# Optimization experiments

Measured on AMD Instinct MI355X. Metric: run time of the kernel, lower is better.

Reference implementation:

```python
import jax, jax.numpy as jnp
import numpy as np

B, C, H, W = 4, 64, 160, 160
OUT = 64
KS = (5, 7)


def conv2d(x, w, b=None, pad=0, groups=1):
    y = jax.lax.conv_general_dilated(
        x, w, (1, 1), [(pad, pad), (pad, pad)],
        feature_group_count=groups,
        dimension_numbers=('NCHW', 'OIHW', 'NCHW'))
    return y if b is None else y + b[None, :, None, None]


def bn_eval(x, g, b, m, v, eps=1e-5):
    s = g / jnp.sqrt(v + eps)
    return x * s[None, :, None, None] + (b - m * s)[None, :, None, None]


def boundary_attn(x, w1, b1, w2, b2):
    Cc = x.shape[1]
    kx = jnp.array([[-1., 0., 1.], [-2., 0., 2.], [-1., 0., 1.]], jnp.float32)
    ky = jnp.array([[-1., -2., -1.], [0., 0., 0.], [1., 2., 1.]], jnp.float32)
    sobel = jnp.concatenate([jnp.tile(kx[None, None], (Cc, 1, 1, 1)),
                             jnp.tile(ky[None, None], (Cc, 1, 1, 1))], axis=0)  # [2C,1,3,3]
    # grouped conv (groups=C): same output-channel grouping semantics as torch
    edge = jnp.abs(conv2d(x, sobel, pad=1, groups=Cc))
    edge = (edge[:, :Cc] + edge[:, Cc:]).mean(axis=1, keepdims=True)
    a = jax.nn.relu(conv2d(x, w1, b1, pad=1))
    a = conv2d(a, w2, b2, pad=0)
    a = jax.nn.sigmoid(a + edge)
    return x * a + x


def icc(off, half_k):
    # iterative cumulative constraint over the (small, static) K channel axis
    K = off.shape[1]
    cs = [None] * K
    cs[half_k] = off[:, half_k]
    for i in range(1, half_k + 1):
        cs[half_k - i] = 0.5 * cs[half_k - i + 1] + 0.5 * off[:, half_k - i]
        cs[half_k + i] = 0.5 * cs[half_k + i - 1] + 0.5 * off[:, half_k + i]
    c = jnp.stack(cs, axis=1)
    w = jnp.ones((K, 1, 3, 3), jnp.float32) / 9.0
    return conv2d(c, w, pad=1, groups=K)


def tumor_center(x):
    _, _, Hx, Wx = x.shape
    fs = x.mean(axis=1)  # [B,H,W]
    hg = jnp.arange(Hx, dtype=x.dtype)[None, :, None]
    wg = jnp.arange(Wx, dtype=x.dtype)[None, None, :]
    tot = fs.sum(axis=(1, 2)) + 1e-6
    return (fs * hg).sum(axis=(1, 2)) / tot, (fs * wg).sum(axis=(1, 2)) / tot


def dyn1d(x, kw, kb, K, O):
    # Original Dynamic1DConv reshapes x to [B*H*W, C, 1, 1] and grid_samples a
    # [1,K] grid per pixel. With align_corners=True a 1x1 input maps every grid
    # coordinate to ix=iy=0, so sampled[n,c,k] == x[b,c,h,w] for all k; the
    # bmm with per-pixel kernels followed by sum over C therefore collapses to
    # (sum_c x) * (sum_k kernels) -- same math, no giant gather materialized.
    Bx, _, Hx, Wx = x.shape
    ker = conv2d(x, kw, kb, pad=0).reshape(Bx, O, K, Hx, Wx)
    return x.sum(axis=1, keepdims=True) * ker.sum(axis=2)


def reference(x, ba_w1, ba_b1, ba_w2, ba_b2,
              off_w1, off_b1, off_bn_g, off_bn_b, off_bn_m, off_bn_v,
              off_w2, off_b2,
              rk5_w, rk5_b, rk7_w, rk7_b,
              lk5_w, lk5_b, lk7_w, lk7_b,
              sf_w, sf_b, sf_bn_g, sf_bn_b, sf_bn_m, sf_bn_v,
              fc_w, fc_b):
    residual = x  # in_channels == out_channels -> nn.Identity
    xa = boundary_attn(x, ba_w1, ba_b1, ba_w2, ba_b2)
    # offset branch (faithful to original; mathematically dead because the
    # per-pixel grid_sample ignores its grid -- see dyn1d). BN in eval mode.
    raw = conv2d(xa, off_w1, off_b1, pad=1)
    raw = jax.nn.relu(bn_eval(raw, off_bn_g, off_bn_b, off_bn_m, off_bn_v))
    raw = conv2d(raw, off_w2, off_b2, pad=1)
    sumk, idx = sum(KS), 0
    _offs = []
    for k in KS:
        _offs.append(icc(jnp.tanh(raw[:, idx:idx + k]), k // 2))
        _offs.append(icc(jnp.tanh(raw[:, sumk + idx:sumk + idx + k]), k // 2))
        idx += k
    _hc, _wc = tumor_center(xa)  # also dead w.r.t. output
    O = OUT // 2 // len(KS)  # 16 channels per scale per flow type
    feats = [dyn1d(xa, rk5_w, rk5_b, 5, O), dyn1d(xa, rk7_w, rk7_b, 7, O),
             dyn1d(xa, lk5_w, lk5_b, 5, O), dyn1d(xa, lk7_w, lk7_b, 7, O)]
    fusion = jnp.concatenate(feats, axis=1)  # [B, OUT, H, W]
    y = jax.nn.relu(bn_eval(conv2d(fusion, sf_w, sf_b, pad=1),
                            sf_bn_g, sf_bn_b, sf_bn_m, sf_bn_v))
    y = conv2d(y, fc_w, fc_b, pad=0)
    return y + residual


def setup_inputs() -> dict:
    key = jax.random.key(0)
    keys = iter(jax.random.split(key, 40))
    def nrm(shape, s=0.05):
        return jax.random.normal(next(keys), shape, jnp.float32) * s
    d = {}
    d['x'] = nrm((B, C, H, W), 1.0)
    d['ba_w1'] = nrm((C // 2, C, 3, 3)); d['ba_b1'] = nrm((C // 2,))
    d['ba_w2'] = nrm((1, C // 2, 1, 1)); d['ba_b2'] = nrm((1,))
    d['off_w1'] = nrm((C // 2, C, 3, 3)); d['off_b1'] = nrm((C // 2,))
    d['off_bn_g'] = 1.0 + nrm((C // 2,)); d['off_bn_b'] = nrm((C // 2,))
    d['off_bn_m'] = nrm((C // 2,))
    d['off_bn_v'] = jax.random.uniform(next(keys), (C // 2,), jnp.float32, 0.5, 1.5)
    d['off_w2'] = nrm((2 * sum(KS), C // 2, 3, 3)); d['off_b2'] = nrm((2 * sum(KS),))
    O = OUT // 2 // len(KS)
    for name, k in (('rk5', 5), ('rk7', 7), ('lk5', 5), ('lk7', 7)):
        d[name + '_w'] = nrm((O * k, C, 1, 1)); d[name + '_b'] = nrm((O * k,))
    d['sf_w'] = nrm((OUT, OUT, 3, 3)); d['sf_b'] = nrm((OUT,))
    d['sf_bn_g'] = 1.0 + nrm((OUT,)); d['sf_bn_b'] = nrm((OUT,))
    d['sf_bn_m'] = nrm((OUT,))
    d['sf_bn_v'] = jax.random.uniform(next(keys), (OUT,), jnp.float32, 0.5, 1.5)
    d['fc_w'] = nrm((OUT, OUT, 1, 1)); d['fc_b'] = nrm((OUT,))
    return d
```

## Files before the change

kernel.cpp:

```cpp
#include <hip/hip_runtime.h>
#include <hip/hip_bf16.h>
#include <math.h>

#define BB 4
#define CC 64
#define HH 160
#define WW 160
#define HWs (HH*WW)
#define NPIX (BB*HWs)

using bf16 = __hip_bfloat16;
typedef __attribute__((ext_vector_type(8)))  short short8v;
typedef __attribute__((ext_vector_type(16))) float float16v;

__device__ __forceinline__ unsigned short f2bfu(float f){
    union { bf16 h; unsigned short u; } cv; cv.h = __float2bfloat16(f); return cv.u;
}
__device__ __forceinline__ float bfu2f(unsigned short u){
    union { float f; unsigned int i; } cv; cv.i = ((unsigned int)u)<<16; return cv.f;
}
__device__ __forceinline__ float16v fzero16(){
    float16v z;
    #pragma unroll
    for(int i=0;i<16;i++) z[i]=0.f;
    return z;
}

constexpr int B1X1 = 0;
constexpr int SFBo = 64;
constexpr int SFWf = 128;
constexpr int BAWf = 18560;
constexpr int FUWf = 27776;
constexpr int FCWf = 29824;
constexpr int WS_FLOATS = 31872;

__global__ void k_prep(const float* __restrict__ rk5w, const float* __restrict__ rk5b,
                       const float* __restrict__ rk7w, const float* __restrict__ rk7b,
                       const float* __restrict__ lk5w, const float* __restrict__ lk5b,
                       const float* __restrict__ lk7w, const float* __restrict__ lk7b,
                       const float* __restrict__ sfw,  const float* __restrict__ sfb,
                       const float* __restrict__ bng,  const float* __restrict__ bnb,
                       const float* __restrict__ bnm,  const float* __restrict__ bnv,
                       const float* __restrict__ baw1, const float* __restrict__ fcw,
                       float* __restrict__ ws)
{
    int tid = blockIdx.x*blockDim.x + threadIdx.x;
    int nt  = gridDim.x*blockDim.x;
    for(int o=tid;o<64;o+=nt){
        int grp=o>>4, oo=o&15; int K=(grp&1)?7:5;
        const float* bp = (grp==0)?rk5b:(grp==1)?rk7b:(grp==2)?lk5b:lk7b;
        float s=0.f; for(int k=0;k<K;k++) s += bp[oo*K+k];
        ws[B1X1+o]=s;
    }
    for(int oc=tid;oc<64;oc+=nt){
        float sc = bng[oc]*rsqrtf(bnv[oc]+1e-5f);
        ws[SFBo+oc] = sfb[oc]*sc + bnb[oc] - bnm[oc]*sc;
    }
    unsigned short* sfwf = (unsigned short*)(ws + SFWf);
    for(int idx=tid; idx<36864; idx+=nt){
        int og = idx/18432;  int rem = idx - og*18432;
        int f  = rem>>9;     int r2 = rem & 511;
        int lane = r2>>3;    int j = r2&7;
        int tap = f>>2, kc = f&3;
        int oc = og*32 + (lane&31);
        int ic = kc*16 + (lane>>5)*8 + j;
        float sc = bng[oc]*rsqrtf(bnv[oc]+1e-5f);
        sfwf[idx] = f2bfu(sfw[(oc*64+ic)*9 + tap] * sc);
    }
    unsigned short* bawf = (unsigned short*)(ws + BAWf);
    for(int idx=tid; idx<18432; idx+=nt){
        int f  = idx>>9;     int r2 = idx & 511;
        int lane = r2>>3;    int j = r2&7;
        int tap = f>>2, kc = f&3;
        int oc = lane&31;
        int ic = kc*16 + (lane>>5)*8 + j;
        bawf[idx] = f2bfu(baw1[(oc*64+ic)*9 + tap]);
    }
    unsigned short* fuwf = (unsigned short*)(ws + FUWf);
    for(int idx=tid; idx<4096; idx+=nt){
        int og   = idx>>11;
        int kc   = (idx>>9)&3;
        int lane = (idx>>3)&63;
        int j    = idx&7;
        int oc = og*32 + (lane&31);
        int c  = kc*16 + (lane>>5)*8 + j;
        int grp = oc>>4, oo = oc&15; int K = (grp&1)?7:5;
        const float* w = (grp==0)?rk5w:(grp==1)?rk7w:(grp==2)?lk5w:lk7w;
        float s = 0.f;
        for(int k=0;k<K;k++) s += w[(oo*K+k)*64 + c];
        fuwf[idx] = f2bfu(s);
    }
    unsigned short* fcwf = (unsigned short*)(ws + FCWf);
    for(int idx=tid; idx<4096; idx+=nt){
        int og   = idx>>11;
        int kc   = (idx>>9)&3;
        int lane = (idx>>3)&63;
        int j    = idx&7;
        int oc = og*32 + (lane&31);
        int c  = kc*16 + (lane>>5)*8 + j;
        fcwf[idx] = f2bfu(fcw[oc*64 + c]);
    }
}

__global__ __launch_bounds__(256)
void k_x2nhwc(const float* __restrict__ x, unsigned short* __restrict__ xb)
{
    __shared__ unsigned short ls[128*72];
    const int t = threadIdx.x;
    const int p0 = blockIdx.x*128;
    const int b = p0 / HWs, pp0 = p0 % HWs;
    const float4* xb4 = (const float4*)(x + (size_t)b*CC*HWs + pp0);
    #pragma unroll
    for(int iter=0; iter<8; iter++){
        int idx = iter*256 + t;
        int c = idx>>5, g = idx&31;
        float4 v = xb4[(size_t)c*(HWs/4) + g];
        int px = g*4;
        int bs = (c>>3) ^ ((g>>1)&7);
        unsigned short* base = ls + bs*8 + (c&7);
        base[(px+0)*72] = f2bfu(v.x);
        base[(px+1)*72] = f2bfu(v.y);
        base[(px+2)*72] = f2bfu(v.z);
        base[(px+3)*72] = f2bfu(v.w);
    }
    __syncthreads();
    #pragma unroll
    for(int iter=0; iter<4; iter++){
        int idx = iter*256 + t;
        int sub = idx&7, px = idx>>3;
        int bs = sub ^ ((px>>3)&7);
        short8v v = *(short8v*)(ls + px*72 + bs*8);
        *(short8v*)(xb + ((size_t)(p0+px))*64 + sub*8) = v;
    }
}

__global__ __launch_bounds__(512, 4)
void k_fuse(const unsigned short* __restrict__ xb, const float* __restrict__ bab1,
            const float* __restrict__ baw2, const float* __restrict__ bab2,
            const float* __restrict__ ws, const float* __restrict__ fcb,
            const float* __restrict__ x, float* __restrict__ out)
{
    __shared__ unsigned short xt[240*72];
    __shared__ unsigned short ftile[180*72];
    __shared__ float ebuf[2][180];
    const int bw = blockIdx.x, bh = blockIdx.y, b = blockIdx.z;
    const int t = threadIdx.x;
    const int wave = t>>6, lane = t&63;
    const int half = lane>>5, n = lane&31;
    const int w0 = bw*16, h0 = bh*8;

    const unsigned short* fb = xb + (size_t)b*HWs*64;
    for(int idx=t; idx<1920; idx+=512){
        int sub = idx&7; int pix = idx>>3;
        int r = pix/20, c = pix - r*20;
        int gh = h0-2+r, gw = w0-2+c;
        short8v v = {0,0,0,0,0,0,0,0};
        if(gh>=0&&gh<HH&&gw>=0&&gw<WW)
            v = *(const short8v*)(fb + ((size_t)(gh*WW+gw))*64 + sub*8);
        *(short8v*)(xt + pix*72 + sub*8) = v;
    }
    __syncthreads();

    float cz = 0.f, sx = 0.f;
    if(wave < 6){
        int p = wave*32 + n; if(p > 179) p = 179;
        int pr = p/18, pc = p - pr*18;
        const unsigned short* bawf = (const unsigned short*)(ws + BAWf);
        float16v acc = fzero16();
        #pragma unroll
        for(int kc=0; kc<4; kc++){
            short8v af[9];
            #pragma unroll
            for(int tap=0; tap<9; tap++)
                af[tap] = *(const short8v*)(bawf + (((size_t)(tap*4+kc))*64 + lane)*8);
            #pragma unroll
            for(int tap=0; tap<9; tap++){
                const int dh = tap/3, dw = tap%3;
                short8v bf = *(const short8v*)(xt + ((pr+dh)*20 + pc+dw)*72
                                               + kc*16 + half*8);
                acc = __builtin_amdgcn_mfma_f32_32x32x16_bf16(af[tap], bf, acc, 0,0,0);
            }
        }
        #pragma unroll
        for(int r=0;r<16;r++){
            int oc = (r&3) + 8*(r>>2) + 4*half;
            cz += fmaxf(acc[r]+bab1[oc],0.f)*baw2[oc];
        }
        cz += __shfl_xor(cz, 32);
        short8v ones;
        #pragma unroll
        for(int j=0;j<8;j++) ones[j] = (short)0x3F80;
        float16v s = fzero16();
        #pragma unroll
        for(int kc=0; kc<4; kc++){
            short8v bf = *(const short8v*)(xt + ((pr+1)*20 + pc+1)*72 + kc*16 + half*8);
            s = __builtin_amdgcn_mfma_f32_32x32x16_bf16(ones, bf, s, 0,0,0);
        }
        sx = s[0];
    }
    {
        const int i2 = 511 - t;
        if(i2 < 360){
            const int hf = (i2>=180) ? 1 : 0;
            const int px2 = i2 - hf*180;
            const int r = px2/18, c = px2 - (px2/18)*18;
            float e = 0.f;
            #pragma unroll
            for(int s=0; s<4; s++){
                const int sub = hf*4 + s;
                if(hf==0){
                    short8v a0 = *(const short8v*)(xt + ((r  )*20 + c  )*72 + sub*8);
                    short8v a2 = *(const short8v*)(xt + ((r  )*20 + c+2)*72 + sub*8);
                    short8v a3 = *(const short8v*)(xt + ((r+1)*20 + c  )*72 + sub*8);
                    short8v a5 = *(const short8v*)(xt + ((r+1)*20 + c+2)*72 + sub*8);
                    short8v a6 = *(const short8v*)(xt + ((r+2)*20 + c  )*72 + sub*8);
                    short8v a8 = *(const short8v*)(xt + ((r+2)*20 + c+2)*72 + sub*8);
                    #pragma unroll
                    for(int j=0;j<8;j++){
                        float gx = (bfu2f((unsigned short)a2[j]) - bfu2f((unsigned short)a0[j]))
                           + 2.f*(bfu2f((unsigned short)a5[j]) - bfu2f((unsigned short)a3[j]))
                           +      (bfu2f((unsigned short)a8[j]) - bfu2f((unsigned short)a6[j]));
                        e += fabsf(gx);
                    }
                } else {
                    short8v b0 = *(const short8v*)(xt + ((r  )*20 + c  )*72 + sub*8);
                    short8v b1 = *(const short8v*)(xt + ((r  )*20 + c+1)*72 + sub*8);
                    short8v b2 = *(const short8v*)(xt + ((r  )*20 + c+2)*72 + sub*8);
                    short8v b6 = *(const short8v*)(xt + ((r+2)*20 + c  )*72 + sub*8);
                    short8v b7 = *(const short8v*)(xt + ((r+2)*20 + c+1)*72 + sub*8);
                    short8v b8 = *(const short8v*)(xt + ((r+2)*20 + c+2)*72 + sub*8);
                    #pragma unroll
                    for(int j=0;j<8;j++){
                        float gy = (bfu2f((unsigned short)b6[j]) - bfu2f((unsigned short)b0[j]))
                           + 2.f*(bfu2f((unsigned short)b7[j]) - bfu2f((unsigned short)b1[j]))
                           +      (bfu2f((unsigned short)b2[j]) - bfu2f((unsigned short)b2[j]))*0.f
                           +      (bfu2f((unsigned short)b8[j]) - bfu2f((unsigned short)b2[j]));
                        e += fabsf(gy);
                    }
                }
            }
            ebuf[hf][px2] = e;
        }
    }
    __syncthreads();

    if(wave < 6){
        const unsigned short* fuwf = (const unsigned short*)(ws + FUWf);
        int p0g = wave*32 + n;
        bool wr = (p0g < 180);
        int p = wr ? p0g : 179;
        int pr = p/18, pc = p - pr*18;
        float z = cz + bab2[0] + (ebuf[0][p] + ebuf[1][p]) * (1.f/32.f);
        float A = 1.f + 1.f/(1.f+__expf(-z));
        float Q = A * sx;
        float P = A * Q;
        #pragma unroll
        for(int og=0; og<2; og++){
            float16v a = fzero16();
            #pragma unroll
            for(int kc=0; kc<4; kc++){
                short8v wf = *(const short8v*)(fuwf + (((size_t)og*4 + kc)*64 + lane)*8);
                short8v bf = *(const short8v*)(xt + ((pr+1)*20 + pc+1)*72 + kc*16 + half*8);
                a = __builtin_amdgcn_mfma_f32_32x32x16_bf16(wf, bf, a, 0,0,0);
            }
            float bq[16];
            #pragma unroll
            for(int r=0;r<16;r++) bq[r] = ws[B1X1 + og*32 + (r&3)+8*(r>>2)+4*half];
            unsigned short* base = ftile + p*72 + og*32 + 4*half;
            #pragma unroll
            for(int gq=0; gq<4; gq++){
                union { unsigned long long u; unsigned short s[4]; } pk;
                #pragma unroll
                for(int rr=0; rr<4; rr++)
                    pk.s[rr] = f2bfu(P*a[4*gq+rr] + Q*bq[4*gq+rr]);
                if(wr) *(unsigned long long*)(base + 8*gq) = pk.u;
            }
        }
    }
    __syncthreads();

    const int rp  = wave & 3;
    const int og  = wave >> 2;
    const int row = 2*rp + (n>>4), col = n&15;
    const unsigned short* sfwf = (const unsigned short*)(ws + SFWf);
    const unsigned short* fcwf = (const unsigned short*)(ws + FCWf);

    float16v Y = fzero16();
    #pragma unroll
    for(int kc=0; kc<4; kc++){
        short8v af[9];
        #pragma unroll
        for(int tap=0; tap<9; tap++)
            af[tap] = *(const short8v*)(sfwf + (((size_t)og*36 + tap*4+kc)*64 + lane)*8);
        #pragma unroll
        for(int tap=0; tap<9; tap++){
            const int dh = tap/3, dw = tap%3;
            short8v bf = *(const short8v*)(ftile + ((row+dh)*18 + col+dw)*72
                                           + kc*16 + half*8);
            Y = __builtin_amdgcn_mfma_f32_32x32x16_bf16(af[tap], bf, Y, 0,0,0);
        }
    }
    unsigned short yb[16];
    #pragma unroll
    for(int r=0;r<16;r++){
        float bias = ws[SFBo + og*32 + (r&3)+8*(r>>2)+4*half];
        yb[r] = f2bfu(fmaxf(Y[r] + bias, 0.f));
    }
    unsigned long long* ybx64 = (unsigned long long*)xt;
    if(og==1){
        #pragma unroll
        for(int q=0;q<4;q++){
            union { unsigned long long u; unsigned short s[4]; } pk;
            #pragma unroll
            for(int rr=0;rr<4;rr++) pk.s[rr] = yb[4*q+rr];
            ybx64[((size_t)rp*64 + lane)*4 + q] = pk.u;
        }
    }
    __syncthreads();
    if(og==0){
        float16v F0 = fzero16(), F1 = fzero16();
        #pragma unroll
        for(int kcl=0; kcl<2; kcl++){
            unsigned short l0,l1,l2,l3, s0,s1,s2,s3;
            if(half==0){ l0=yb[8*kcl+0]; l1=yb[8*kcl+1]; l2=yb[8*kcl+2]; l3=yb[8*kcl+3];
                         s0=yb[8*kcl+4]; s1=yb[8*kcl+5]; s2=yb[8*kcl+6]; s3=yb[8*kcl+7]; }
            else       { l0=yb[8*kcl+4]; l1=yb[8*kcl+5]; l2=yb[8*kcl+6]; l3=yb[8*kcl+7];
                         s0=yb[8*kcl+0]; s1=yb[8*kcl+1]; s2=yb[8*kcl+2]; s3=yb[8*kcl+3]; }
            int p0 = (int)((unsigned)s0 | ((unsigned)s1<<16));
            int p1 = (int)((unsigned)s2 | ((unsigned)s3<<16));
            int r0 = __shfl_xor(p0, 32);
            int r1 = __shfl_xor(p1, 32);
            unsigned short m0 = (unsigned short)(r0 & 0xffff);
            unsigned short m1 = (unsigned short)(((unsigned)r0) >> 16);
            unsigned short m2 = (unsigned short)(r1 & 0xffff);
            unsigned short m3 = (unsigned short)(((unsigned)r1) >> 16);
            short8v B;
            if(half==0){ B[0]=(short)l0; B[1]=(short)l1; B[2]=(short)l2; B[3]=(short)l3;
                         B[4]=(short)m0; B[5]=(short)m1; B[6]=(short)m2; B[7]=(short)m3; }
            else       { B[0]=(short)m0; B[1]=(short)m1; B[2]=(short)m2; B[3]=(short)m3;
                         B[4]=(short)l0; B[5]=(short)l1; B[6]=(short)l2; B[7]=(short)l3; }
            short8v fa0 = *(const short8v*)(fcwf + (((size_t)0*4 + kcl)*64 + lane)*8);
            short8v fa1 = *(const short8v*)(fcwf + (((size_t)1*4 + kcl)*64 + lane)*8);
            F0 = __builtin_amdgcn_mfma_f32_32x32x16_bf16(fa0, B, F0, 0,0,0);
            F1 = __builtin_amdgcn_mfma_f32_32x32x16_bf16(fa1, B, F1, 0,0,0);
        }
        #pragma unroll
        for(int kcl=0; kcl<2; kcl++){
            const int kc_fc = 2 + kcl;
            const int gsel  = 2*kcl + half;
            const int srcA  = half ? (lane^32) : lane;
            const int srcB  = half ? lane : (lane^32);
            unsigned long long a03 = ybx64[((size_t)rp*64 + srcA)*4 + gsel];
            unsigned long long a47 = ybx64[((size_t)rp*64 + srcB)*4 + gsel];
            short8v B;
            #pragma unroll
            for(int j2=0;j2<4;j2++){
                B[j2]   = (short)(unsigned short)((a03 >> (16*j2)) & 0xffff);
                B[4+j2] = (short)(unsigned short)((a47 >> (16*j2)) & 0xffff);
            }
            short8v fa0 = *(const short8v*)(fcwf + (((size_t)0*4 + kc_fc)*64 + lane)*8);
            short8v fa1 = *(const short8v*)(fcwf + (((size_t)1*4 + kc_fc)*64 + lane)*8);
            F0 = __builtin_amdgcn_mfma_f32_32x32x16_bf16(fa0, B, F0, 0,0,0);
            F1 = __builtin_amdgcn_mfma_f32_32x32x16_bf16(fa1, B, F1, 0,0,0);
        }
        #pragma unroll
        for(int og2=0; og2<2; og2++){
            #pragma unroll
            for(int r=0;r<16;r++){
                int oc = og2*32 + (r&3)+8*(r>>2)+4*half;
                size_t g = ((size_t)(b*CC + oc))*HWs + (h0+row)*WW + w0 + col;
                float v = (og2==0) ? F0[r] : F1[r];
                out[g] = v + fcb[oc] + x[g];
            }
        }
    }
}

extern "C" void kernel_launch(void* const* d_in, const int* in_sizes, int n_in,
                              void* d_out, int out_size, void* d_ws, size_t ws_size,
                              hipStream_t stream)
{
    const float* x     = (const float*)d_in[0];
    const float* ba_w1 = (const float*)d_in[1];
    const float* ba_b1 = (const float*)d_in[2];
    const float* ba_w2 = (const float*)d_in[3];
    const float* ba_b2 = (const float*)d_in[4];
    const float* rk5_w = (const float*)d_in[13];
    const float* rk5_b = (const float*)d_in[14];
    const float* rk7_w = (const float*)d_in[15];
    const float* rk7_b = (const float*)d_in[16];
    const float* lk5_w = (const float*)d_in[17];
    const float* lk5_b = (const float*)d_in[18];
    const float* lk7_w = (const float*)d_in[19];
    const float* lk7_b = (const float*)d_in[20];
    const float* sf_w  = (const float*)d_in[21];
    const float* sf_b  = (const float*)d_in[22];
    const float* bng   = (const float*)d_in[23];
    const float* bnb   = (const float*)d_in[24];
    const float* bnm   = (const float*)d_in[25];
    const float* bnv   = (const float*)d_in[26];
    const float* fc_w  = (const float*)d_in[27];
    const float* fc_b  = (const float*)d_in[28];

    float* wsf = (float*)d_ws;
    unsigned short* XB  = (unsigned short*)((char*)d_ws + (size_t)WS_FLOATS*4);
    float* out = (float*)d_out;

    k_prep<<<64, 256, 0, stream>>>(rk5_w,rk5_b,rk7_w,rk7_b,lk5_w,lk5_b,lk7_w,lk7_b,
                                   sf_w,sf_b,bng,bnb,bnm,bnv, ba_w1, fc_w, wsf);
    k_x2nhwc<<<NPIX/128, 256, 0, stream>>>(x, XB);
    k_fuse<<<dim3(10,20,4), 512, 0, stream>>>(XB, ba_b1, ba_w2, ba_b2, wsf, fc_b, x, out);
}
```

Before: 174.0 us.

## Shrink k_fuse shared memory by aliasing tiles into xt to raise occupancy

Removes the separate ftile and ebuf shared buffers. The edge sums and fused features are written into the already-loaded xt tile, overwriting center pixels and using padding slots, and the exchange buffer is split into two smaller halves with extra barriers. Launch bounds are raised from 4 to 8 blocks per CU so more workgroups can be resident. In exchange, overwriting xt in place requires the earlier reads to finish first, and the extra syncs and tighter register budget could cause spills.

```diff
diff --git a/kernel.cpp b/kernel.cpp
--- a/kernel.cpp
+++ b/kernel.cpp
@@ -134,15 +134,14 @@
     }
 }
 
-__global__ __launch_bounds__(512, 4)
+__global__ __launch_bounds__(512, 8)
 void k_fuse(const unsigned short* __restrict__ xb, const float* __restrict__ bab1,
             const float* __restrict__ baw2, const float* __restrict__ bab2,
             const float* __restrict__ ws, const float* __restrict__ fcb,
             const float* __restrict__ x, float* __restrict__ out)
 {
     __shared__ unsigned short xt[240*72];
-    __shared__ unsigned short ftile[180*72];
-    __shared__ float ebuf[2][180];
+    __shared__ unsigned long long ybex[4*64*2];
     const int bw = blockIdx.x, bh = blockIdx.y, b = blockIdx.z;
     const int t = threadIdx.x;
     const int wave = t>>6, lane = t&63;
@@ -233,13 +232,13 @@
                     for(int j=0;j<8;j++){
                         float gy = (bfu2f((unsigned short)b6[j]) - bfu2f((unsigned short)b0[j]))
                            + 2.f*(bfu2f((unsigned short)b7[j]) - bfu2f((unsigned short)b1[j]))
-                           +      (bfu2f((unsigned short)b2[j]) - bfu2f((unsigned short)b2[j]))*0.f
                            +      (bfu2f((unsigned short)b8[j]) - bfu2f((unsigned short)b2[j]));
                         e += fabsf(gy);
                     }
                 }
             }
-            ebuf[hf][px2] = e;
+            float* ep = (float*)(xt + px2*72 + 64);
+            ep[hf] = e;
         }
     }
     __syncthreads();
@@ -250,10 +249,12 @@
         bool wr = (p0g < 180);
         int p = wr ? p0g : 179;
         int pr = p/18, pc = p - pr*18;
-        float z = cz + bab2[0] + (ebuf[0][p] + ebuf[1][p]) * (1.f/32.f);
+        const float* ep = (const float*)(xt + p*72 + 64);
+        float z = cz + bab2[0] + (ep[0] + ep[1]) * (1.f/32.f);
         float A = 1.f + 1.f/(1.f+__expf(-z));
         float Q = A * sx;
         float P = A * Q;
+        unsigned long long pk8[8];
         #pragma unroll
         for(int og=0; og<2; og++){
             float16v a = fzero16();
@@ -266,14 +267,23 @@
             float bq[16];
             #pragma unroll
             for(int r=0;r<16;r++) bq[r] = ws[B1X1 + og*32 + (r&3)+8*(r>>2)+4*half];
-            unsigned short* base = ftile + p*72 + og*32 + 4*half;
             #pragma unroll
             for(int gq=0; gq<4; gq++){
                 union { unsigned long long u; unsigned short s[4]; } pk;
                 #pragma unroll
                 for(int rr=0; rr<4; rr++)
                     pk.s[rr] = f2bfu(P*a[4*gq+rr] + Q*bq[4*gq+rr]);
-                if(wr) *(unsigned long long*)(base + 8*gq) = pk.u;
+                pk8[og*4+gq] = pk.u;
+            }
+        }
+        if(wr){
+            unsigned short* cen = xt + ((pr+1)*20 + pc+1)*72;
+            #pragma unroll
+            for(int og=0; og<2; og++){
+                unsigned short* b2 = cen + og*32 + 4*half;
+                #pragma unroll
+                for(int gq=0; gq<4; gq++)
+                    *(unsigned long long*)(b2 + 8*gq) = pk8[og*4+gq];
             }
         }
     }
@@ -295,7 +305,7 @@
         #pragma unroll
         for(int tap=0; tap<9; tap++){
             const int dh = tap/3, dw = tap%3;
-            short8v bf = *(const short8v*)(ftile + ((row+dh)*18 + col+dw)*72
+            short8v bf = *(const short8v*)(xt + ((row+dh+1)*20 + (col+dw+1))*72
                                            + kc*16 + half*8);
             Y = __builtin_amdgcn_mfma_f32_32x32x16_bf16(af[tap], bf, Y, 0,0,0);
         }
@@ -306,19 +316,18 @@
         float bias = ws[SFBo + og*32 + (r&3)+8*(r>>2)+4*half];
         yb[r] = f2bfu(fmaxf(Y[r] + bias, 0.f));
     }
-    unsigned long long* ybx64 = (unsigned long long*)xt;
     if(og==1){
         #pragma unroll
-        for(int q=0;q<4;q++){
+        for(int q=0;q<2;q++){
             union { unsigned long long u; unsigned short s[4]; } pk;
             #pragma unroll
             for(int rr=0;rr<4;rr++) pk.s[rr] = yb[4*q+rr];
-            ybx64[((size_t)rp*64 + lane)*4 + q] = pk.u;
-        }
-    }
-    __syncthreads();
+            ybex[((size_t)rp*64 + lane)*2 + q] = pk.u;
+        }
+    }
+    __syncthreads();
+    float16v F0 = fzero16(), F1 = fzero16();
     if(og==0){
-        float16v F0 = fzero16(), F1 = fzero16();
         #pragma unroll
         for(int kcl=0; kcl<2; kcl++){
             unsigned short l0,l1,l2,l3, s0,s1,s2,s3;
@@ -344,22 +353,48 @@
             F0 = __builtin_amdgcn_mfma_f32_32x32x16_bf16(fa0, B, F0, 0,0,0);
             F1 = __builtin_amdgcn_mfma_f32_32x32x16_bf16(fa1, B, F1, 0,0,0);
         }
-        #pragma unroll
-        for(int kcl=0; kcl<2; kcl++){
-            const int kc_fc = 2 + kcl;
-            const int gsel  = 2*kcl + half;
+        {
             const int srcA  = half ? (lane^32) : lane;
             const int srcB  = half ? lane : (lane^32);
-            unsigned long long a03 = ybx64[((size_t)rp*64 + srcA)*4 + gsel];
-            unsigned long long a47 = ybx64[((size_t)rp*64 + srcB)*4 + gsel];
+            unsigned long long a03 = ybex[((size_t)rp*64 + srcA)*2 + half];
+            unsigned long long a47 = ybex[((size_t)rp*64 + srcB)*2 + half];
             short8v B;
             #pragma unroll
             for(int j2=0;j2<4;j2++){
                 B[j2]   = (short)(unsigned short)((a03 >> (16*j2)) & 0xffff);
                 B[4+j2] = (short)(unsigned short)((a47 >> (16*j2)) & 0xffff);
             }
-            short8v fa0 = *(const short8v*)(fcwf + (((size_t)0*4 + kc_fc)*64 + lane)*8);
-            short8v fa1 = *(const short8v*)(fcwf + (((size_t)1*4 + kc_fc)*64 + lane)*8);
+            short8v fa0 = *(const short8v*)(fcwf + (((size_t)0*4 + 2)*64 + lane)*8);
+            short8v fa1 = *(const short8v*)(fcwf + (((size_t)1*4 + 2)*64 + lane)*8);
+            F0 = __builtin_amdgcn_mfma_f32_32x32x16_bf16(fa0, B, F0, 0,0,0);
+            F1 = __builtin_amdgcn_mfma_f32_32x32x16_bf16(fa1, B, F1, 0,0,0);
+        }
+    }
+    __syncthreads();
+    if(og==1){
+        #pragma unroll
+        for(int q=0;q<2;q++){
+            union { unsigned long long u; unsigned short s[4]; } pk;
+            #pragma unroll
+            for(int rr=0;rr<4;rr++) pk.s[rr] = yb[4*(q+2)+rr];
+            ybex[((size_t)rp*64 + lane)*2 + q] = pk.u;
+        }
+    }
+    __syncthreads();
+    if(og==0){
+        {
+            const int srcA  = half ? (lane^32) : lane;
+            const int srcB  = half ? lane : (lane^32);
+            unsigned long long a03 = ybex[((size_t)rp*64 + srcA)*2 + half];
+            unsigned long long a47 = ybex[((size_t)rp*64 + srcB)*2 + half];
+            short8v B;
+            #pragma unroll
+            for(int j2=0;j2<4;j2++){
+                B[j2]   = (short)(unsigned short)((a03 >> (16*j2)) & 0xffff);
+                B[4+j2] = (short)(unsigned short)((a47 >> (16*j2)) & 0xffff);
+            }
+            short8v fa0 = *(const short8v*)(fcwf + (((size_t)0*4 + 3)*64 + lane)*8);
+            short8v fa1 = *(const short8v*)(fcwf + (((size_t)1*4 + 3)*64 + lane)*8);
             F0 = __builtin_amdgcn_mfma_f32_32x32x16_bf16(fa0, B, F0, 0,0,0);
             F1 = __builtin_amdgcn_mfma_f32_32x32x16_bf16(fa1, B, F1, 0,0,0);
         }
```

Measured after the change: 185.2 us. +6.5%, slower.
